# Kernel optimization log

Measured on AMD Instinct MI355X. Metric: run time of the kernel, lower is better.

The kernel has to match this reference:

```python
import jax, jax.numpy as jnp
import numpy as np


def _maxpool2x2(t):
    # t: [B, H, W, C] -> [B, H//2, W//2, C], 2x2 max pool stride 2
    B, H, W, C = t.shape
    return t.reshape(B, H // 2, 2, W // 2, 2, C).max(axis=(2, 4))


def setup_inputs() -> dict:
    key = jax.random.key(0)
    ks = jax.random.split(key, 7)
    B, H, W, C = 16, 64, 64, 256
    x = jax.random.normal(ks[0], (B, H, W, C), jnp.float32)
    w_theta = jax.random.normal(ks[1], (C, C // 8), jnp.float32) * 0.05
    w_phi = jax.random.normal(ks[2], (C, C // 8), jnp.float32) * 0.05
    w_g = jax.random.normal(ks[3], (C, C // 2), jnp.float32) * 0.05
    w_o = jax.random.normal(ks[4], (C // 2, C), jnp.float32) * 0.05
    b_o = jnp.zeros((C,), jnp.float32)
    sigma = jax.random.normal(ks[5], (), jnp.float32)
    return {"x": x, "w_theta": w_theta, "w_phi": w_phi, "w_g": w_g,
            "w_o": w_o, "b_o": b_o, "sigma": sigma}


def reference(x, w_theta, w_phi, w_g, w_o, b_o, sigma):
    B, H, W, C = x.shape
    L = H * W          # location_num = 4096
    Ld = L // 4        # downsampled_num (after 2x2 maxpool)
    # 1x1 convs == channel GEMMs
    theta = jnp.einsum('bhwc,cd->bhwd', x, w_theta).reshape(B, L, C // 8)
    phi = jnp.einsum('bhwc,cd->bhwd', x, w_phi)
    phi = _maxpool2x2(phi).reshape(B, Ld, C // 8)
    attn = jax.nn.softmax(jnp.einsum('bld,bmd->blm', theta, phi), axis=-1)  # [B, L, Ld]
    g = jnp.einsum('bhwc,cd->bhwd', x, w_g)
    g = _maxpool2x2(g).reshape(B, Ld, C // 2)
    attn_g = jnp.einsum('blm,bmd->bld', attn, g).reshape(B, H, W, C // 2)
    attn_g = jnp.einsum('bhwd,dc->bhwc', attn_g, w_o) + b_o
    return x + sigma * attn_g
```

## Files before the change

kernel.cpp:

```cpp
#include <hip/hip_runtime.h>
#include <hip/hip_bf16.h>


typedef __attribute__((ext_vector_type(8))) short bf16x8;
typedef __attribute__((ext_vector_type(4))) short bf16x4;
typedef __attribute__((ext_vector_type(4))) float f32x4;

#define MFMA16(A,B,C) __builtin_amdgcn_mfma_f32_16x16x32_bf16(A,B,C,0,0,0)

#define GLOAD16(GSRC, LDST)                                                        \
    __builtin_amdgcn_global_load_lds(                                              \
        (const __attribute__((address_space(1))) unsigned int*)(GSRC),             \
        (__attribute__((address_space(3))) unsigned int*)(LDST), 16, 0, 0)

static __device__ __forceinline__ unsigned short f2b(float f) {
    __hip_bfloat16 h = __float2bfloat16(f);
    return *reinterpret_cast<unsigned short*>(&h);
}
static __device__ __forceinline__ float blo(unsigned int u){ return __uint_as_float(u << 16); }
static __device__ __forceinline__ float bhi(unsigned int u){ return __uint_as_float(u & 0xffff0000u); }

__global__ void k_prep(const float* __restrict__ w_theta, const float* __restrict__ w_phi,
                       const float* __restrict__ w_g, const float* __restrict__ w_o,
                       unsigned short* __restrict__ WT, unsigned short* __restrict__ woT)
{
    int bid = blockIdx.x, t = threadIdx.x;
    if (bid < 192) {
        int n = bid;
        float v;
        if (n < 32)      v = w_theta[t * 32 + n];
        else if (n < 64) v = w_phi[t * 32 + (n - 32)];
        else             v = w_g[t * 128 + (n - 64)];
        WT[n * 256 + t] = f2b(v);
    } else if (t < 128) {
        int cc = bid - 192;
        woT[cc * 128 + t] = f2b(w_o[t * 256 + cc]);
    }
}

__global__ __launch_bounds__(256) void k_proj(
    const float* __restrict__ x, const unsigned short* __restrict__ WT,
    unsigned short* __restrict__ theta_b, unsigned short* __restrict__ phi_b,
    unsigned short* __restrict__ g_b)
{
    __shared__ unsigned short xT[128 * 64];
    __shared__ unsigned short wT[192 * 64];
    const int t = threadIdx.x;
    const int w = t >> 6, l = t & 63, G = l >> 4, c = l & 15;
    const size_t row0 = (size_t)blockIdx.x * 128;

    f32x4 acc[2][12];
#pragma unroll
    for (int i = 0; i < 2; i++)
#pragma unroll
        for (int j = 0; j < 12; j++) acc[i][j] = (f32x4){0.f, 0.f, 0.f, 0.f};

    for (int k0 = 0; k0 < 256; k0 += 64) {
        __syncthreads();
#pragma unroll
        for (int it = 0; it < 4; it++) {
            int u = it * 256 + t, r = u >> 3, s = u & 7;
            const float* px = x + (row0 + r) * 256 + k0 + s * 8;
            float4 a = *(const float4*)px;
            float4 bq = *(const float4*)(px + 4);
            uint4 v;
            v.x = (unsigned)f2b(a.x) | ((unsigned)f2b(a.y) << 16);
            v.y = (unsigned)f2b(a.z) | ((unsigned)f2b(a.w) << 16);
            v.z = (unsigned)f2b(bq.x) | ((unsigned)f2b(bq.y) << 16);
            v.w = (unsigned)f2b(bq.z) | ((unsigned)f2b(bq.w) << 16);
            *(uint4*)((char*)xT + r * 128 + ((s * 16) ^ ((r & 7) << 4))) = v;
        }
#pragma unroll
        for (int it = 0; it < 6; it++) {
            int u = it * 256 + t, r = u >> 3, s = u & 7;
            uint4 v = *(const uint4*)(WT + r * 256 + k0 + s * 8);
            *(uint4*)((char*)wT + r * 128 + ((s * 16) ^ ((r & 7) << 4))) = v;
        }
        __syncthreads();
#pragma unroll
        for (int kin = 0; kin < 2; kin++) {
            int m0r = (2 * w) * 16 + c, m1r = (2 * w + 1) * 16 + c;
            bf16x8 a0 = *(const bf16x8*)((char*)xT + m0r * 128 + ((kin * 64 + G * 16) ^ ((m0r & 7) << 4)));
            bf16x8 a1 = *(const bf16x8*)((char*)xT + m1r * 128 + ((kin * 64 + G * 16) ^ ((m1r & 7) << 4)));
#pragma unroll
            for (int nt = 0; nt < 12; nt++) {
                int nr = nt * 16 + c;
                bf16x8 bv = *(const bf16x8*)((char*)wT + nr * 128 + ((kin * 64 + G * 16) ^ ((nr & 7) << 4)));
                acc[0][nt] = MFMA16(a0, bv, acc[0][nt]);
                acc[1][nt] = MFMA16(a1, bv, acc[1][nt]);
            }
        }
    }
#pragma unroll
    for (int mt = 0; mt < 2; mt++)
#pragma unroll
        for (int nt = 0; nt < 12; nt++)
#pragma unroll
            for (int i = 0; i < 4; i++) {
                size_t row = row0 + (2 * w + mt) * 16 + 4 * G + i;
                unsigned short v = f2b(acc[mt][nt][i]);
                if (nt < 2)      theta_b[row * 32 + nt * 16 + c] = v;
                else if (nt < 4) phi_b[row * 32 + (nt - 2) * 16 + c] = v;
                else             g_b[row * 128 + (nt - 4) * 16 + c] = v;
            }
}

__global__ __launch_bounds__(256) void k_pool(
    const unsigned short* __restrict__ phi_b, const unsigned short* __restrict__ g_b,
    unsigned short* __restrict__ phi_p, unsigned short* __restrict__ g_pT)
{
    const int bid = blockIdx.x, t = threadIdx.x;
    if (bid < 1024) {
        const unsigned int* p32 = (const unsigned int*)phi_b;
        unsigned int* pp32 = (unsigned int*)phi_p;
        int idx = bid * 256 + t;
        int b = idx >> 14, r = idx & 16383, pm = r >> 4, d2 = r & 15;
        int hp = pm >> 5, wp = pm & 31;
        size_t base = ((size_t)b * 4096 + (2 * hp) * 64 + 2 * wp) * 16 + d2;
        unsigned v0 = p32[base], v1 = p32[base + 16], v2 = p32[base + 1024], v3 = p32[base + 1040];
        float lo = fmaxf(fmaxf(blo(v0), blo(v1)), fmaxf(blo(v2), blo(v3)));
        float hi = fmaxf(fmaxf(bhi(v0), bhi(v1)), fmaxf(bhi(v2), bhi(v3)));
        pp32[(idx & ~15) | (d2 ^ ((pm & 3) << 2))] =
            (unsigned)f2b(lo) | ((unsigned)f2b(hi) << 16);
    } else {
        __shared__ unsigned short P[32 * 128];
        int b = (bid - 1024) >> 5, hp = (bid - 1024) & 31;
        const unsigned int* g32 = (const unsigned int*)g_b;
#pragma unroll
        for (int it = 0; it < 8; it++) {
            int u = it * 256 + t, wp = u >> 6, d2 = u & 63;
            size_t base = ((size_t)b * 4096 + (2 * hp) * 64 + 2 * wp) * 64 + d2;
            unsigned v0 = g32[base], v1 = g32[base + 64], v2 = g32[base + 4096], v3 = g32[base + 4160];
            float lo = fmaxf(fmaxf(blo(v0), blo(v1)), fmaxf(blo(v2), blo(v3)));
            float hi = fmaxf(fmaxf(bhi(v0), bhi(v1)), fmaxf(bhi(v2), bhi(v3)));
            unsigned pv = (unsigned)f2b(lo) | ((unsigned)f2b(hi) << 16);
            *(unsigned*)((char*)P + wp * 256 + ((d2 * 4) ^ ((wp & 7) << 4))) = pv;
        }
        __syncthreads();
#pragma unroll
        for (int it = 0; it < 2; it++) {
            int d = t & 127, s4 = (t >> 7) + it * 2;
            union { unsigned short v[8]; uint4 q; } pk;
#pragma unroll
            for (int k = 0; k < 8; k++) {
                int wp = s4 * 8 + k;
                pk.v[k] = *(const unsigned short*)((char*)P + wp * 256 + ((d * 2) ^ ((wp & 7) << 4)));
            }
            int midx = (hp * 32 + s4 * 8) ^ ((d & 7) << 3);
            *(uint4*)(g_pT + ((size_t)b * 128 + d) * 1024 + midx) = pk.q;
        }
    }
}

__global__ __launch_bounds__(128, 2) void k_attn(
    const unsigned short* __restrict__ theta_b, const unsigned short* __restrict__ phi_p,
    const unsigned short* __restrict__ g_pT, const unsigned short* __restrict__ woT,
    const float* __restrict__ x, const float* __restrict__ b_o,
    const float* __restrict__ sigma_p, float* __restrict__ out)
{
    __shared__ char lds[40960];

    const int t = threadIdx.x;
    const int w = t >> 6, l = t & 63, G = l >> 4, c = l & 15;
    const int bid = (blockIdx.x & 7) * 128 + (blockIdx.x >> 3);
    const int b = bid >> 6;
    const int q0 = (bid & 63) * 64;
    const int xr = (c & 7) << 4;
    const int xr3 = (c & 3) << 4;

    const unsigned short* gsrc_base = g_pT + (size_t)b * 131072;
    const unsigned short* psrc_base = phi_p + (size_t)b * 32768;
#define STAGE(BI, MCN)                                                                  \
    {                                                                                   \
        char* gb = lds + (BI) * 20480;                                                  \
        char* pb = gb + 16384;                                                          \
        _Pragma("unroll")                                                               \
        for (int it = 0; it < 8; it++) {                                                \
            int d = (it * 128 + t) >> 3, s = t & 7;                                     \
            GLOAD16(gsrc_base + (size_t)d * 1024 + (MCN) * 64 + s * 8,                  \
                    gb + it * 2048 + w * 1024);                                         \
        }                                                                               \
        _Pragma("unroll")                                                               \
        for (int it = 0; it < 2; it++) {                                                \
            int u = it * 128 + t, r = u >> 2, s = u & 3;                                \
            GLOAD16(psrc_base + (size_t)((MCN) * 64 + r) * 32 + s * 8,                  \
                    pb + it * 2048 + w * 1024);                                         \
        }                                                                               \
    }

    STAGE(0, 0);
    {
        char* th = lds + 36864;
#pragma unroll
        for (int it = 0; it < 2; it++) {
            int u = it * 128 + t, r = u >> 2, s = u & 3;
            uint4 v = *(const uint4*)(theta_b + ((size_t)(b * 4096 + q0 + r)) * 32 + s * 8);
            *(uint4*)(th + r * 64 + ((s * 16) ^ ((r & 3) << 4))) = v;
        }
    }
    __syncthreads();

    bf16x8 bt0, bt1;
    {
        const char* th = lds + 36864;
        bt0 = *(const bf16x8*)(th + (w * 32 + c) * 64 + ((G * 16) ^ xr3));
        bt1 = *(const bf16x8*)(th + (w * 32 + 16 + c) * 64 + ((G * 16) ^ xr3));
    }
    __syncthreads();

    f32x4 oacc[2][8];
#pragma unroll
    for (int qt = 0; qt < 2; qt++)
#pragma unroll
        for (int dt = 0; dt < 8; dt++) oacc[qt][dt] = (f32x4){0.f, 0.f, 0.f, 0.f};
    float ps[2] = {0.f, 0.f};
    const f32x4 zf = (f32x4){0.f, 0.f, 0.f, 0.f};

    for (int mc = 0; mc < 16; mc++) {
        const int cur = mc & 1;
        if (mc < 15) {
            STAGE(cur ^ 1, mc + 1);
            asm volatile("s_waitcnt vmcnt(10)" ::: "memory");
        } else {
            asm volatile("s_waitcnt vmcnt(0)" ::: "memory");
        }
        __builtin_amdgcn_sched_barrier(0);
        __builtin_amdgcn_s_barrier();
        __builtin_amdgcn_sched_barrier(0);

        const char* gL   = lds + cur * 20480;
        const char* phiL = gL + 16384;

        bf16x8 ap[4];
#pragma unroll
        for (int mt = 0; mt < 4; mt++)
            ap[mt] = *(const bf16x8*)(phiL + (mt * 16 + c) * 64 + ((G * 16) ^ xr3));
        f32x4 sacc[2][4];
        __builtin_amdgcn_s_setprio(1);
#pragma unroll
        for (int mt = 0; mt < 4; mt++) {
            sacc[0][mt] = MFMA16(ap[mt], bt0, zf);
            sacc[1][mt] = MFMA16(ap[mt], bt1, zf);
        }
        __builtin_amdgcn_s_setprio(0);

        bf16x8 pa[2][2];
#pragma unroll
        for (int qt = 0; qt < 2; qt++) {
#pragma unroll
            for (int ks = 0; ks < 2; ks++) {
                union { unsigned u[4]; bf16x8 v; } pu;
#pragma unroll
                for (int hf = 0; hf < 2; hf++) {
                    int mt = 2 * ks + hf;
                    float p0 = __expf(sacc[qt][mt][0]);
                    float p1 = __expf(sacc[qt][mt][1]);
                    float p2 = __expf(sacc[qt][mt][2]);
                    float p3 = __expf(sacc[qt][mt][3]);
                    ps[qt] += (p0 + p1) + (p2 + p3);
                    pu.u[hf * 2]     = (unsigned)f2b(p0) | ((unsigned)f2b(p1) << 16);
                    pu.u[hf * 2 + 1] = (unsigned)f2b(p2) | ((unsigned)f2b(p3) << 16);
                }
                pa[qt][ks] = pu.v;
            }
        }

        __builtin_amdgcn_s_setprio(1);
#pragma unroll
        for (int ks = 0; ks < 2; ks++) {
#pragma unroll
            for (int dt = 0; dt < 8; dt++) {
                const char* rb = gL + (dt * 16 + c) * 128;
                bf16x4 x0 = *(const bf16x4*)(rb + ((64 * ks + 8 * G) ^ xr));
                bf16x4 x1 = *(const bf16x4*)(rb + ((64 * ks + 32 + 8 * G) ^ xr));
                bf16x8 bg = __builtin_shufflevector(x0, x1, 0, 1, 2, 3, 4, 5, 6, 7);
                oacc[0][dt] = MFMA16(pa[0][ks], bg, oacc[0][dt]);
                oacc[1][dt] = MFMA16(pa[1][ks], bg, oacc[1][dt]);
            }
        }
        __builtin_amdgcn_s_setprio(0);

        asm volatile("s_waitcnt lgkmcnt(0)" ::: "memory");
        __builtin_amdgcn_sched_barrier(0);
        __builtin_amdgcn_s_barrier();
        __builtin_amdgcn_sched_barrier(0);
    }
#undef STAGE

#pragma unroll
    for (int qt = 0; qt < 2; qt++) {
        ps[qt] += __shfl_xor(ps[qt], 16);
        ps[qt] += __shfl_xor(ps[qt], 32);
    }
    float rinv[2][4];
#pragma unroll
    for (int qt = 0; qt < 2; qt++)
#pragma unroll
        for (int i = 0; i < 4; i++)
            rinv[qt][i] = 1.0f / __shfl(ps[qt], 4 * G + i);

    char* O_l = lds;
#pragma unroll
    for (int qt = 0; qt < 2; qt++)
#pragma unroll
        for (int dt = 0; dt < 8; dt++)
#pragma unroll
            for (int i = 0; i < 4; i++) {
                int q = w * 32 + qt * 16 + 4 * G + i, d = dt * 16 + c;
                *(unsigned short*)(O_l + q * 256 + ((d * 2) ^ ((q & 7) << 4))) =
                    f2b(oacc[qt][dt][i] * rinv[qt][i]);
            }

    const float sg = *sigma_p;
    char* wo_l = lds + 20480;
    const int arow0 = (w * 32 + c) * 256;
    const int arow1 = (w * 32 + 16 + c) * 256;

    for (int cb = 0; cb < 4; cb++) {
        __syncthreads();
#pragma unroll
        for (int it = 0; it < 8; it++) {
            int u = it * 128 + t, r = u >> 4, s = u & 15;
            uint4 v = *(const uint4*)(woT + (size_t)(cb * 64 + r) * 128 + s * 8);
            *(uint4*)(wo_l + r * 256 + ((s * 16) ^ ((r & 7) << 4))) = v;
        }
        __syncthreads();
        f32x4 eacc[2][4];
#pragma unroll
        for (int qt = 0; qt < 2; qt++)
#pragma unroll
            for (int ct = 0; ct < 4; ct++) eacc[qt][ct] = (f32x4){0.f, 0.f, 0.f, 0.f};
#pragma unroll
        for (int ks = 0; ks < 4; ks++) {
            bf16x8 a0 = *(const bf16x8*)(O_l + arow0 + ((ks * 64 + G * 16) ^ xr));
            bf16x8 a1 = *(const bf16x8*)(O_l + arow1 + ((ks * 64 + G * 16) ^ xr));
#pragma unroll
            for (int ct = 0; ct < 4; ct++) {
                int cr = ct * 16 + c;
                bf16x8 bw = *(const bf16x8*)(wo_l + cr * 256 + ((ks * 64 + G * 16) ^ xr));
                eacc[0][ct] = MFMA16(a0, bw, eacc[0][ct]);
                eacc[1][ct] = MFMA16(a1, bw, eacc[1][ct]);
            }
        }
#pragma unroll
        for (int qt = 0; qt < 2; qt++)
#pragma unroll
            for (int ct = 0; ct < 4; ct++) {
                int col = cb * 64 + ct * 16 + c;
                float bo = b_o[col];
#pragma unroll
                for (int i = 0; i < 4; i++) {
                    size_t off = ((size_t)(b * 4096 + q0 + w * 32 + qt * 16 + 4 * G + i)) * 256 + col;
                    out[off] = x[off] + sg * (eacc[qt][ct][i] + bo);
                }
            }
    }
}

extern "C" void kernel_launch(void* const* d_in, const int* in_sizes, int n_in,
                              void* d_out, int out_size, void* d_ws, size_t ws_size,
                              hipStream_t stream)
{
    const float* x       = (const float*)d_in[0];
    const float* w_theta = (const float*)d_in[1];
    const float* w_phi   = (const float*)d_in[2];
    const float* w_g     = (const float*)d_in[3];
    const float* w_o     = (const float*)d_in[4];
    const float* b_o     = (const float*)d_in[5];
    const float* sigma   = (const float*)d_in[6];
    float* out = (float*)d_out;

    char* ws = (char*)d_ws;
    unsigned short* theta_b = (unsigned short*)(ws);
    unsigned short* phi_b   = (unsigned short*)(ws + 4194304);
    unsigned short* g_b     = (unsigned short*)(ws + 8388608);
    unsigned short* phi_p   = (unsigned short*)(ws + 25165824);
    unsigned short* g_pT    = (unsigned short*)(ws + 26214400);
    unsigned short* WT      = (unsigned short*)(ws + 30408704);
    unsigned short* woT     = (unsigned short*)(ws + 30507008);

    hipLaunchKernelGGL(k_prep, dim3(448), dim3(256), 0, stream,
                       w_theta, w_phi, w_g, w_o, WT, woT);
    hipLaunchKernelGGL(k_proj, dim3(512), dim3(256), 0, stream,
                       x, WT, theta_b, phi_b, g_b);
    hipLaunchKernelGGL(k_pool, dim3(1536), dim3(256), 0, stream,
                       phi_b, g_b, phi_p, g_pT);
    hipLaunchKernelGGL(k_attn, dim3(1024), dim3(128), 0, stream,
                       theta_b, phi_p, g_pT, woT, x, b_o, sigma, out);
}
```

Baseline: 81.81 us.

## Split attention query tile across four waves instead of two

The attention kernel now runs 256 threads per block, with each wave owning 16 query rows instead of 32. The cooperative load loops for g, phi, theta and w_o are redistributed across the larger block, and the wait count is adjusted to match. Per-thread accumulators halve, which lowers register pressure and raises the occupancy bound. The cost is that each wave reuses every LDS-staged g and w_o fragment for half as many MFMAs, so LDS read traffic per MFMA doubles.

```diff
diff --git a/kernel.cpp b/kernel.cpp
--- a/kernel.cpp
+++ b/kernel.cpp
@@ -152,7 +152,7 @@
     }
 }
 
-__global__ __launch_bounds__(128, 2) void k_attn(
+__global__ __launch_bounds__(256, 4) void k_attn(
     const unsigned short* __restrict__ theta_b, const unsigned short* __restrict__ phi_p,
     const unsigned short* __restrict__ g_pT, const unsigned short* __restrict__ woT,
     const float* __restrict__ x, const float* __restrict__ b_o,
@@ -175,52 +175,41 @@
         char* gb = lds + (BI) * 20480;                                                  \
         char* pb = gb + 16384;                                                          \
         _Pragma("unroll")                                                               \
-        for (int it = 0; it < 8; it++) {                                                \
-            int d = (it * 128 + t) >> 3, s = t & 7;                                     \
+        for (int it = 0; it < 4; it++) {                                                \
+            int d = 32 * it + 8 * w + (l >> 3), s = l & 7;                              \
             GLOAD16(gsrc_base + (size_t)d * 1024 + (MCN) * 64 + s * 8,                  \
-                    gb + it * 2048 + w * 1024);                                         \
+                    gb + it * 4096 + w * 1024);                                         \
         }                                                                               \
-        _Pragma("unroll")                                                               \
-        for (int it = 0; it < 2; it++) {                                                \
-            int u = it * 128 + t, r = u >> 2, s = u & 3;                                \
+        {                                                                               \
+            int r = 16 * w + (l >> 2), s = l & 3;                                       \
             GLOAD16(psrc_base + (size_t)((MCN) * 64 + r) * 32 + s * 8,                  \
-                    pb + it * 2048 + w * 1024);                                         \
+                    pb + w * 1024);                                                     \
         }                                                                               \
     }
 
     STAGE(0, 0);
     {
         char* th = lds + 36864;
-#pragma unroll
-        for (int it = 0; it < 2; it++) {
-            int u = it * 128 + t, r = u >> 2, s = u & 3;
-            uint4 v = *(const uint4*)(theta_b + ((size_t)(b * 4096 + q0 + r)) * 32 + s * 8);
-            *(uint4*)(th + r * 64 + ((s * 16) ^ ((r & 3) << 4))) = v;
-        }
+        int r = t >> 2, s = t & 3;
+        uint4 v = *(const uint4*)(theta_b + ((size_t)(b * 4096 + q0 + r)) * 32 + s * 8);
+        *(uint4*)(th + r * 64 + ((s * 16) ^ ((r & 3) << 4))) = v;
     }
     __syncthreads();
 
-    bf16x8 bt0, bt1;
-    {
-        const char* th = lds + 36864;
-        bt0 = *(const bf16x8*)(th + (w * 32 + c) * 64 + ((G * 16) ^ xr3));
-        bt1 = *(const bf16x8*)(th + (w * 32 + 16 + c) * 64 + ((G * 16) ^ xr3));
-    }
+    const bf16x8 bt = *(const bf16x8*)(lds + 36864 + (w * 16 + c) * 64 + ((G * 16) ^ xr3));
     __syncthreads();
 
-    f32x4 oacc[2][8];
-#pragma unroll
-    for (int qt = 0; qt < 2; qt++)
-#pragma unroll
-        for (int dt = 0; dt < 8; dt++) oacc[qt][dt] = (f32x4){0.f, 0.f, 0.f, 0.f};
-    float ps[2] = {0.f, 0.f};
+    f32x4 oacc[8];
+#pragma unroll
+    for (int dt = 0; dt < 8; dt++) oacc[dt] = (f32x4){0.f, 0.f, 0.f, 0.f};
+    float ps = 0.f;
     const f32x4 zf = (f32x4){0.f, 0.f, 0.f, 0.f};
 
     for (int mc = 0; mc < 16; mc++) {
         const int cur = mc & 1;
         if (mc < 15) {
             STAGE(cur ^ 1, mc + 1);
-            asm volatile("s_waitcnt vmcnt(10)" ::: "memory");
+            asm volatile("s_waitcnt vmcnt(5)" ::: "memory");
         } else {
             asm volatile("s_waitcnt vmcnt(0)" ::: "memory");
         }
@@ -235,34 +224,28 @@
 #pragma unroll
         for (int mt = 0; mt < 4; mt++)
             ap[mt] = *(const bf16x8*)(phiL + (mt * 16 + c) * 64 + ((G * 16) ^ xr3));
-        f32x4 sacc[2][4];
+        f32x4 sacc[4];
         __builtin_amdgcn_s_setprio(1);
 #pragma unroll
-        for (int mt = 0; mt < 4; mt++) {
-            sacc[0][mt] = MFMA16(ap[mt], bt0, zf);
-            sacc[1][mt] = MFMA16(ap[mt], bt1, zf);
-        }
+        for (int mt = 0; mt < 4; mt++) sacc[mt] = MFMA16(ap[mt], bt, zf);
         __builtin_amdgcn_s_setprio(0);
 
-        bf16x8 pa[2][2];
-#pragma unroll
-        for (int qt = 0; qt < 2; qt++) {
-#pragma unroll
-            for (int ks = 0; ks < 2; ks++) {
-                union { unsigned u[4]; bf16x8 v; } pu;
-#pragma unroll
-                for (int hf = 0; hf < 2; hf++) {
-                    int mt = 2 * ks + hf;
-                    float p0 = __expf(sacc[qt][mt][0]);
-                    float p1 = __expf(sacc[qt][mt][1]);
-                    float p2 = __expf(sacc[qt][mt][2]);
-                    float p3 = __expf(sacc[qt][mt][3]);
-                    ps[qt] += (p0 + p1) + (p2 + p3);
-                    pu.u[hf * 2]     = (unsigned)f2b(p0) | ((unsigned)f2b(p1) << 16);
-                    pu.u[hf * 2 + 1] = (unsigned)f2b(p2) | ((unsigned)f2b(p3) << 16);
-                }
-                pa[qt][ks] = pu.v;
-            }
+        bf16x8 pa[2];
+#pragma unroll
+        for (int ks = 0; ks < 2; ks++) {
+            union { unsigned u[4]; bf16x8 v; } pu;
+#pragma unroll
+            for (int hf = 0; hf < 2; hf++) {
+                int mt = 2 * ks + hf;
+                float p0 = __expf(sacc[mt][0]);
+                float p1 = __expf(sacc[mt][1]);
+                float p2 = __expf(sacc[mt][2]);
+                float p3 = __expf(sacc[mt][3]);
+                ps += (p0 + p1) + (p2 + p3);
+                pu.u[hf * 2]     = (unsigned)f2b(p0) | ((unsigned)f2b(p1) << 16);
+                pu.u[hf * 2 + 1] = (unsigned)f2b(p2) | ((unsigned)f2b(p3) << 16);
+            }
+            pa[ks] = pu.v;
         }
 
         __builtin_amdgcn_s_setprio(1);
@@ -274,8 +257,7 @@
                 bf16x4 x0 = *(const bf16x4*)(rb + ((64 * ks + 8 * G) ^ xr));
                 bf16x4 x1 = *(const bf16x4*)(rb + ((64 * ks + 32 + 8 * G) ^ xr));
                 bf16x8 bg = __builtin_shufflevector(x0, x1, 0, 1, 2, 3, 4, 5, 6, 7);
-                oacc[0][dt] = MFMA16(pa[0][ks], bg, oacc[0][dt]);
-                oacc[1][dt] = MFMA16(pa[1][ks], bg, oacc[1][dt]);
+                oacc[dt] = MFMA16(pa[ks], bg, oacc[dt]);
             }
         }
         __builtin_amdgcn_s_setprio(0);
@@ -287,73 +269,57 @@
     }
 #undef STAGE
 
-#pragma unroll
-    for (int qt = 0; qt < 2; qt++) {
-        ps[qt] += __shfl_xor(ps[qt], 16);
-        ps[qt] += __shfl_xor(ps[qt], 32);
-    }
-    float rinv[2][4];
-#pragma unroll
-    for (int qt = 0; qt < 2; qt++)
-#pragma unroll
-        for (int i = 0; i < 4; i++)
-            rinv[qt][i] = 1.0f / __shfl(ps[qt], 4 * G + i);
+    ps += __shfl_xor(ps, 16);
+    ps += __shfl_xor(ps, 32);
+    float rinv[4];
+#pragma unroll
+    for (int i = 0; i < 4; i++) rinv[i] = 1.0f / __shfl(ps, 4 * G + i);
 
     char* O_l = lds;
 #pragma unroll
-    for (int qt = 0; qt < 2; qt++)
-#pragma unroll
-        for (int dt = 0; dt < 8; dt++)
-#pragma unroll
-            for (int i = 0; i < 4; i++) {
-                int q = w * 32 + qt * 16 + 4 * G + i, d = dt * 16 + c;
-                *(unsigned short*)(O_l + q * 256 + ((d * 2) ^ ((q & 7) << 4))) =
-                    f2b(oacc[qt][dt][i] * rinv[qt][i]);
-            }
+    for (int dt = 0; dt < 8; dt++)
+#pragma unroll
+        for (int i = 0; i < 4; i++) {
+            int row = w * 16 + 4 * G + i, d = dt * 16 + c;
+            *(unsigned short*)(O_l + row * 256 + ((d * 2) ^ ((row & 7) << 4))) =
+                f2b(oacc[dt][i] * rinv[i]);
+        }
 
     const float sg = *sigma_p;
     char* wo_l = lds + 20480;
-    const int arow0 = (w * 32 + c) * 256;
-    const int arow1 = (w * 32 + 16 + c) * 256;
+    const int arow = (w * 16 + c) * 256;
 
     for (int cb = 0; cb < 4; cb++) {
         __syncthreads();
 #pragma unroll
-        for (int it = 0; it < 8; it++) {
-            int u = it * 128 + t, r = u >> 4, s = u & 15;
+        for (int it = 0; it < 4; it++) {
+            int u = it * 256 + t, r = u >> 4, s = u & 15;
             uint4 v = *(const uint4*)(woT + (size_t)(cb * 64 + r) * 128 + s * 8);
             *(uint4*)(wo_l + r * 256 + ((s * 16) ^ ((r & 7) << 4))) = v;
         }
         __syncthreads();
-        f32x4 eacc[2][4];
-#pragma unroll
-        for (int qt = 0; qt < 2; qt++)
-#pragma unroll
-            for (int ct = 0; ct < 4; ct++) eacc[qt][ct] = (f32x4){0.f, 0.f, 0.f, 0.f};
+        f32x4 eacc[4];
+#pragma unroll
+        for (int ct = 0; ct < 4; ct++) eacc[ct] = (f32x4){0.f, 0.f, 0.f, 0.f};
 #pragma unroll
         for (int ks = 0; ks < 4; ks++) {
-            bf16x8 a0 = *(const bf16x8*)(O_l + arow0 + ((ks * 64 + G * 16) ^ xr));
-            bf16x8 a1 = *(const bf16x8*)(O_l + arow1 + ((ks * 64 + G * 16) ^ xr));
+            bf16x8 a0 = *(const bf16x8*)(O_l + arow + ((ks * 64 + G * 16) ^ xr));
 #pragma unroll
             for (int ct = 0; ct < 4; ct++) {
-                int cr = ct * 16 + c;
-                bf16x8 bw = *(const bf16x8*)(wo_l + cr * 256 + ((ks * 64 + G * 16) ^ xr));
-                eacc[0][ct] = MFMA16(a0, bw, eacc[0][ct]);
-                eacc[1][ct] = MFMA16(a1, bw, eacc[1][ct]);
-            }
-        }
-#pragma unroll
-        for (int qt = 0; qt < 2; qt++)
-#pragma unroll
-            for (int ct = 0; ct < 4; ct++) {
-                int col = cb * 64 + ct * 16 + c;
-                float bo = b_o[col];
-#pragma unroll
-                for (int i = 0; i < 4; i++) {
-                    size_t off = ((size_t)(b * 4096 + q0 + w * 32 + qt * 16 + 4 * G + i)) * 256 + col;
-                    out[off] = x[off] + sg * (eacc[qt][ct][i] + bo);
-                }
-            }
+                bf16x8 bw = *(const bf16x8*)(wo_l + (ct * 16 + c) * 256 + ((ks * 64 + G * 16) ^ xr));
+                eacc[ct] = MFMA16(a0, bw, eacc[ct]);
+            }
+        }
+#pragma unroll
+        for (int ct = 0; ct < 4; ct++) {
+            int col = cb * 64 + ct * 16 + c;
+            float bo = b_o[col];
+#pragma unroll
+            for (int i = 0; i < 4; i++) {
+                size_t off = ((size_t)(b * 4096 + q0 + w * 16 + 4 * G + i)) * 256 + col;
+                out[off] = x[off] + sg * (eacc[ct][i] + bo);
+            }
+        }
     }
 }
 
@@ -385,6 +351,6 @@
                        x, WT, theta_b, phi_b, g_b);
     hipLaunchKernelGGL(k_pool, dim3(1536), dim3(256), 0, stream,
                        phi_b, g_b, phi_p, g_pT);
-    hipLaunchKernelGGL(k_attn, dim3(1024), dim3(128), 0, stream,
+    hipLaunchKernelGGL(k_attn, dim3(1024), dim3(256), 0, stream,
                        theta_b, phi_p, g_pT, woT, x, b_o, sigma, out);
 }
```

New measurement: 86.47 us. 1.06x slower.

## Double attention block to 128 queries with 4 waves sharing staged phi/g tiles

Applied to the files above, without the earlier changes.

The attention kernel now uses 256-thread blocks covering 128 query rows, so each staged phi and pooled-g chunk in LDS serves four waves instead of two. Grid size and global staging traffic per query drop by half. The pool kernel's transpose permutes key order so that g values can be read as a single 16-byte LDS load instead of two 8-byte loads. The output projection is re-tiled into 32-column chunks with per-wave-pair O buffers to fit in LDS. The cost is a larger block and LDS reuse that may lower occupancy and increase barrier waits.

```diff
diff --git a/kernel.cpp b/kernel.cpp
--- a/kernel.cpp
+++ b/kernel.cpp
@@ -3,7 +3,6 @@
 
 
 typedef __attribute__((ext_vector_type(8))) short bf16x8;
-typedef __attribute__((ext_vector_type(4))) short bf16x4;
 typedef __attribute__((ext_vector_type(4))) float f32x4;
 
 #define MFMA16(A,B,C) __builtin_amdgcn_mfma_f32_16x16x32_bf16(A,B,C,0,0,0)
@@ -143,7 +142,7 @@
             union { unsigned short v[8]; uint4 q; } pk;
 #pragma unroll
             for (int k = 0; k < 8; k++) {
-                int wp = s4 * 8 + k;
+                int wp = 16 * (k >> 2) + 4 * s4 + (k & 3);
                 pk.v[k] = *(const unsigned short*)((char*)P + wp * 256 + ((d * 2) ^ ((wp & 7) << 4)));
             }
             int midx = (hp * 32 + s4 * 8) ^ ((d & 7) << 3);
@@ -152,7 +151,7 @@
     }
 }
 
-__global__ __launch_bounds__(128, 2) void k_attn(
+__global__ __launch_bounds__(256, 4) void k_attn(
     const unsigned short* __restrict__ theta_b, const unsigned short* __restrict__ phi_p,
     const unsigned short* __restrict__ g_pT, const unsigned short* __restrict__ woT,
     const float* __restrict__ x, const float* __restrict__ b_o,
@@ -162,9 +161,9 @@
 
     const int t = threadIdx.x;
     const int w = t >> 6, l = t & 63, G = l >> 4, c = l & 15;
-    const int bid = (blockIdx.x & 7) * 128 + (blockIdx.x >> 3);
-    const int b = bid >> 6;
-    const int q0 = (bid & 63) * 64;
+    const int bid = (blockIdx.x & 7) * 64 + (blockIdx.x >> 3);
+    const int b = bid >> 5;
+    const int q0 = (bid & 31) * 128;
     const int xr = (c & 7) << 4;
     const int xr3 = (c & 3) << 4;
 
@@ -175,25 +174,24 @@
         char* gb = lds + (BI) * 20480;                                                  \
         char* pb = gb + 16384;                                                          \
         _Pragma("unroll")                                                               \
-        for (int it = 0; it < 8; it++) {                                                \
-            int d = (it * 128 + t) >> 3, s = t & 7;                                     \
+        for (int it = 0; it < 4; it++) {                                                \
+            int d = 32 * it + 8 * w + (l >> 3), s = l & 7;                              \
             GLOAD16(gsrc_base + (size_t)d * 1024 + (MCN) * 64 + s * 8,                  \
-                    gb + it * 2048 + w * 1024);                                         \
+                    gb + it * 4096 + w * 1024);                                         \
         }                                                                               \
-        _Pragma("unroll")                                                               \
-        for (int it = 0; it < 2; it++) {                                                \
-            int u = it * 128 + t, r = u >> 2, s = u & 3;                                \
+        {                                                                               \
+            int r = 16 * w + (l >> 2), s = l & 3;                                       \
             GLOAD16(psrc_base + (size_t)((MCN) * 64 + r) * 32 + s * 8,                  \
-                    pb + it * 2048 + w * 1024);                                         \
+                    pb + w * 1024);                                                     \
         }                                                                               \
     }
 
     STAGE(0, 0);
     {
-        char* th = lds + 36864;
+        char* th = lds + 20480;
 #pragma unroll
         for (int it = 0; it < 2; it++) {
-            int u = it * 128 + t, r = u >> 2, s = u & 3;
+            int u = it * 256 + t, r = u >> 2, s = u & 3;
             uint4 v = *(const uint4*)(theta_b + ((size_t)(b * 4096 + q0 + r)) * 32 + s * 8);
             *(uint4*)(th + r * 64 + ((s * 16) ^ ((r & 3) << 4))) = v;
         }
@@ -202,7 +200,7 @@
 
     bf16x8 bt0, bt1;
     {
-        const char* th = lds + 36864;
+        const char* th = lds + 20480;
         bt0 = *(const bf16x8*)(th + (w * 32 + c) * 64 + ((G * 16) ^ xr3));
         bt1 = *(const bf16x8*)(th + (w * 32 + 16 + c) * 64 + ((G * 16) ^ xr3));
     }
@@ -220,7 +218,7 @@
         const int cur = mc & 1;
         if (mc < 15) {
             STAGE(cur ^ 1, mc + 1);
-            asm volatile("s_waitcnt vmcnt(10)" ::: "memory");
+            asm volatile("s_waitcnt vmcnt(5)" ::: "memory");
         } else {
             asm volatile("s_waitcnt vmcnt(0)" ::: "memory");
         }
@@ -246,7 +244,7 @@
 
         bf16x8 pa[2][2];
 #pragma unroll
-        for (int qt = 0; qt < 2; qt++) {
+        for (int qt = 0; qt < 2; qt++)
 #pragma unroll
             for (int ks = 0; ks < 2; ks++) {
                 union { unsigned u[4]; bf16x8 v; } pu;
@@ -263,17 +261,13 @@
                 }
                 pa[qt][ks] = pu.v;
             }
-        }
 
         __builtin_amdgcn_s_setprio(1);
 #pragma unroll
         for (int ks = 0; ks < 2; ks++) {
 #pragma unroll
             for (int dt = 0; dt < 8; dt++) {
-                const char* rb = gL + (dt * 16 + c) * 128;
-                bf16x4 x0 = *(const bf16x4*)(rb + ((64 * ks + 8 * G) ^ xr));
-                bf16x4 x1 = *(const bf16x4*)(rb + ((64 * ks + 32 + 8 * G) ^ xr));
-                bf16x8 bg = __builtin_shufflevector(x0, x1, 0, 1, 2, 3, 4, 5, 6, 7);
+                bf16x8 bg = *(const bf16x8*)(gL + (dt * 16 + c) * 128 + ((64 * ks + 16 * G) ^ xr));
                 oacc[0][dt] = MFMA16(pa[0][ks], bg, oacc[0][dt]);
                 oacc[1][dt] = MFMA16(pa[1][ks], bg, oacc[1][dt]);
             }
@@ -299,45 +293,47 @@
         for (int i = 0; i < 4; i++)
             rinv[qt][i] = 1.0f / __shfl(ps[qt], 4 * G + i);
 
-    char* O_l = lds;
-#pragma unroll
-    for (int qt = 0; qt < 2; qt++)
-#pragma unroll
-        for (int dt = 0; dt < 8; dt++)
-#pragma unroll
-            for (int i = 0; i < 4; i++) {
-                int q = w * 32 + qt * 16 + 4 * G + i, d = dt * 16 + c;
-                *(unsigned short*)(O_l + q * 256 + ((d * 2) ^ ((q & 7) << 4))) =
-                    f2b(oacc[qt][dt][i] * rinv[qt][i]);
-            }
+    {
+        char* O_h = lds + (w >> 1) * 16384;
+#pragma unroll
+        for (int qt = 0; qt < 2; qt++)
+#pragma unroll
+            for (int dt = 0; dt < 8; dt++)
+#pragma unroll
+                for (int i = 0; i < 4; i++) {
+                    int ql = (w & 1) * 32 + qt * 16 + 4 * G + i, d = dt * 16 + c;
+                    *(unsigned short*)(O_h + ql * 256 + ((d * 2) ^ ((ql & 7) << 4))) =
+                        f2b(oacc[qt][dt][i] * rinv[qt][i]);
+                }
+    }
 
     const float sg = *sigma_p;
-    char* wo_l = lds + 20480;
-    const int arow0 = (w * 32 + c) * 256;
-    const int arow1 = (w * 32 + 16 + c) * 256;
-
-    for (int cb = 0; cb < 4; cb++) {
-        __syncthreads();
-#pragma unroll
-        for (int it = 0; it < 8; it++) {
-            int u = it * 128 + t, r = u >> 4, s = u & 15;
-            uint4 v = *(const uint4*)(woT + (size_t)(cb * 64 + r) * 128 + s * 8);
+    const char* O_h = lds + (w >> 1) * 16384;
+    char* wo_l = lds + 32768;
+    const int arow0 = ((w & 1) * 32 + c) * 256;
+    const int arow1 = ((w & 1) * 32 + 16 + c) * 256;
+
+    for (int cb = 0; cb < 8; cb++) {
+        __syncthreads();
+#pragma unroll
+        for (int it = 0; it < 2; it++) {
+            int u = it * 256 + t, r = u >> 4, s = u & 15;
+            uint4 v = *(const uint4*)(woT + (size_t)(cb * 32 + r) * 128 + s * 8);
             *(uint4*)(wo_l + r * 256 + ((s * 16) ^ ((r & 7) << 4))) = v;
         }
         __syncthreads();
-        f32x4 eacc[2][4];
+        f32x4 eacc[2][2];
 #pragma unroll
         for (int qt = 0; qt < 2; qt++)
 #pragma unroll
-            for (int ct = 0; ct < 4; ct++) eacc[qt][ct] = (f32x4){0.f, 0.f, 0.f, 0.f};
+            for (int ct = 0; ct < 2; ct++) eacc[qt][ct] = (f32x4){0.f, 0.f, 0.f, 0.f};
 #pragma unroll
         for (int ks = 0; ks < 4; ks++) {
-            bf16x8 a0 = *(const bf16x8*)(O_l + arow0 + ((ks * 64 + G * 16) ^ xr));
-            bf16x8 a1 = *(const bf16x8*)(O_l + arow1 + ((ks * 64 + G * 16) ^ xr));
-#pragma unroll
-            for (int ct = 0; ct < 4; ct++) {
-                int cr = ct * 16 + c;
-                bf16x8 bw = *(const bf16x8*)(wo_l + cr * 256 + ((ks * 64 + G * 16) ^ xr));
+            bf16x8 a0 = *(const bf16x8*)(O_h + arow0 + ((ks * 64 + G * 16) ^ xr));
+            bf16x8 a1 = *(const bf16x8*)(O_h + arow1 + ((ks * 64 + G * 16) ^ xr));
+#pragma unroll
+            for (int ct = 0; ct < 2; ct++) {
+                bf16x8 bw = *(const bf16x8*)(wo_l + (ct * 16 + c) * 256 + ((ks * 64 + G * 16) ^ xr));
                 eacc[0][ct] = MFMA16(a0, bw, eacc[0][ct]);
                 eacc[1][ct] = MFMA16(a1, bw, eacc[1][ct]);
             }
@@ -345,8 +341,8 @@
 #pragma unroll
         for (int qt = 0; qt < 2; qt++)
 #pragma unroll
-            for (int ct = 0; ct < 4; ct++) {
-                int col = cb * 64 + ct * 16 + c;
+            for (int ct = 0; ct < 2; ct++) {
+                int col = cb * 32 + ct * 16 + c;
                 float bo = b_o[col];
 #pragma unroll
                 for (int i = 0; i < 4; i++) {
@@ -385,6 +381,6 @@
                        x, WT, theta_b, phi_b, g_b);
     hipLaunchKernelGGL(k_pool, dim3(1536), dim3(256), 0, stream,
                        phi_b, g_b, phi_p, g_pT);
-    hipLaunchKernelGGL(k_attn, dim3(1024), dim3(128), 0, stream,
+    hipLaunchKernelGGL(k_attn, dim3(512), dim3(256), 0, stream,
                        theta_b, phi_p, g_pT, woT, x, b_o, sigma, out);
 }
```

New measurement: 112.6 us. +37.6%, slower.
